# Optimization experiments

Hardware: AMD Instinct MI355X
Metric: run time of the kernel (lower is better)

Reference implementation:

```python
import jax, jax.numpy as jnp
import numpy as np

N_HEAD = 16


def setup_inputs() -> dict:
    key = jax.random.key(0)
    ks = jax.random.split(key, 3)
    B, T, C = 4, 2048, 1024
    x = jax.random.normal(ks[0], (B, T, C), dtype=jnp.float32)
    w_attn = jax.random.normal(ks[1], (3 * C, C), dtype=jnp.float32) * (1.0 / np.sqrt(C))
    b_attn = jnp.zeros((3 * C,), dtype=jnp.float32)
    w_proj = jax.random.normal(ks[2], (C, C), dtype=jnp.float32) * (1.0 / np.sqrt(C))
    b_proj = jnp.zeros((C,), dtype=jnp.float32)
    return {"x": x, "w_attn": w_attn, "b_attn": b_attn, "w_proj": w_proj, "b_proj": b_proj}


def reference(x, w_attn, b_attn, w_proj, b_proj):
    B, T, C = x.shape
    H = N_HEAD
    D = C // H
    qkv = x @ w_attn.T + b_attn                      # [B, T, 3C]
    q, k, v = jnp.split(qkv, 3, axis=-1)
    # [B, T, C] -> [B, H, T, D]
    q = q.reshape(B, T, H, D).transpose(0, 2, 1, 3)
    k = k.reshape(B, T, H, D).transpose(0, 2, 1, 3)
    v = v.reshape(B, T, H, D).transpose(0, 2, 1, 3)
    scale = 1.0 / np.sqrt(D).astype(np.float32)
    att = jnp.einsum('bhqd,bhkd->bhqk', q, k) * scale  # [B, H, T, T]
    causal = jnp.tril(jnp.ones((T, T), dtype=bool))
    att = jnp.where(causal[None, None], att, -jnp.inf)
    att = jax.nn.softmax(att, axis=-1)
    y = jnp.einsum('bhqk,bhkd->bhqd', att, v)          # [B, H, T, D]
    y = y.transpose(0, 2, 1, 3).reshape(B, T, C)
    return y @ w_proj.T + b_proj
```

## Files before the change

kernel.cpp:

```cpp
#include <hip/hip_runtime.h>
#include <hip/hip_bf16.h>
#include <stdint.h>

typedef __attribute__((ext_vector_type(8))) short bf16x8;
typedef __attribute__((ext_vector_type(8))) unsigned short ushort8;
typedef __attribute__((ext_vector_type(4))) float f32x4;

#define MFMA16(a, b, c) __builtin_amdgcn_mfma_f32_16x16x32_bf16((a), (b), (c), 0, 0, 0)

__device__ __forceinline__ unsigned short f2bf(float f) {
  unsigned int u = __builtin_bit_cast(unsigned int, f);
  unsigned int r = (u + 0x7fffu + ((u >> 16) & 1u)) >> 16;
  return (unsigned short)r;
}

__device__ __forceinline__ void gload16(const unsigned short* g, unsigned short* lds_dst) {
  __builtin_amdgcn_global_load_lds(
      (const __attribute__((address_space(1))) unsigned int*)g,
      (__attribute__((address_space(3))) unsigned int*)lds_dst, 16, 0, 0);
}

__global__ void cvt_all(const float* __restrict__ x, const float* __restrict__ wa,
                        const float* __restrict__ wp, unsigned short* __restrict__ xb,
                        unsigned short* __restrict__ wab, unsigned short* __restrict__ wpb) {
  const int C0 = 1048576;
  const int C1 = 1441792;
  const int C2 = 1572864;
  int i = blockIdx.x * blockDim.x + threadIdx.x;
  const int stride = gridDim.x * blockDim.x;
  for (; i < C2; i += stride) {
    const float* src; unsigned short* dst; long e;
    if (i < C0)      { src = x;  dst = xb;  e = (long)i * 8; }
    else if (i < C1) { src = wa; dst = wab; e = (long)(i - C0) * 8; }
    else             { src = wp; dst = wpb; e = (long)(i - C1) * 8; }
    float4 v0 = *(const float4*)(src + e);
    float4 v1 = *(const float4*)(src + e + 4);
    ushort8 o;
    o[0] = f2bf(v0.x); o[1] = f2bf(v0.y); o[2] = f2bf(v0.z); o[3] = f2bf(v0.w);
    o[4] = f2bf(v1.x); o[5] = f2bf(v1.y); o[6] = f2bf(v1.z); o[7] = f2bf(v1.w);
    *(ushort8*)(dst + e) = o;
  }
}

template <int EPI, int NB>
__global__ __launch_bounds__(512, 2)
void gemm_bt(const unsigned short* __restrict__ A,
             const unsigned short* __restrict__ Bt,
             const float* __restrict__ bias,
             int M, int N, int K,
             unsigned short* __restrict__ q_out,
             unsigned short* __restrict__ k_out,
             unsigned short* __restrict__ vt_out,
             float* __restrict__ f_out) {
  constexpr int BNT = NB * 64;
  alignas(16) __shared__ unsigned short Alds[2][2][128 * 64];
  alignas(16) __shared__ unsigned short Blds[2][BNT * 64];
  const int t = threadIdx.x, w = t >> 6, l = t & 63;
  const int bm = blockIdx.x, bn = blockIdx.y;
  const int wm = w >> 2, wn = w & 3;
  const int lo = l & 15, hi = l >> 4, swk = lo & 7;

  f32x4 acc[8][NB];
  const f32x4 zero = {0.f, 0.f, 0.f, 0.f};
#pragma unroll
  for (int i = 0; i < 8; ++i)
#pragma unroll
    for (int j = 0; j < NB; ++j) acc[i][j] = zero;

  const int sr = t >> 3;
  const int gsrcE = ((t & 7) ^ (sr & 7)) * 8;
  const unsigned short* Asrc = A + (long)(bm * 256 + sr) * K + gsrcE;
  const unsigned short* Bsrc = Bt + (long)(bn * BNT + sr) * K + gsrcE;

#define STAGE_AH(sb, qh, koff) do {                                    \
    unsigned short* d_ = &Alds[sb][qh][w * 512];                       \
    const unsigned short* s_ = Asrc + (long)(qh) * 64 * K + (koff);    \
    gload16(s_, d_); gload16(s_ + 128L * K, d_ + 4096); } while (0)
#define STAGE_B(sb, koff) do {                                         \
    _Pragma("unroll")                                                  \
    for (int c_ = 0; c_ < NB; ++c_)                                    \
      gload16(Bsrc + (long)c_ * 64 * K + (koff),                       \
              &Blds[sb][c_ * 4096 + w * 512]); } while (0)

  STAGE_AH(0, 0, 0);
  STAGE_B(0, 0);
  STAGE_AH(0, 1, 0);
  asm volatile("s_waitcnt vmcnt(2)" ::: "memory");
  __builtin_amdgcn_sched_barrier(0);
  __builtin_amdgcn_s_barrier();

  const int lrA = (wm * 64 + lo) * 64;
  const int lrB = (wn * (NB * 16) + lo) * 64;
  const int gk0 = ((hi) ^ swk) * 8;
  const int gk1 = ((4 + hi) ^ swk) * 8;

  bf16x8 af[4][2], blo[2][2], bhi[2];

  for (int kt = 0; kt < 16; ++kt) {
    const int c = kt & 1, nb = c ^ 1;
    const bool st = (kt < 15);
    const int koff = (kt + 1) * 64;
    const unsigned short* A0 = Alds[c][0];
    const unsigned short* A1 = Alds[c][1];
    const unsigned short* Bs = Blds[c];

#pragma unroll
    for (int ii = 0; ii < 4; ++ii) {
      af[ii][0] = *(const bf16x8*)&A0[lrA + ii * 1024 + gk0];
      af[ii][1] = *(const bf16x8*)&A0[lrA + ii * 1024 + gk1];
    }
#pragma unroll
    for (int jj = 0; jj < NB - 1; ++jj) {
      blo[jj][0] = *(const bf16x8*)&Bs[lrB + jj * 1024 + gk0];
      blo[jj][1] = *(const bf16x8*)&Bs[lrB + jj * 1024 + gk1];
    }
    if (st) STAGE_AH(nb, 0, koff);
    __builtin_amdgcn_s_barrier();
    asm volatile("s_waitcnt lgkmcnt(0)" ::: "memory");
    __builtin_amdgcn_sched_barrier(0);
    __builtin_amdgcn_s_setprio(1);
#pragma unroll
    for (int ii = 0; ii < 4; ++ii)
#pragma unroll
      for (int jj = 0; jj < NB - 1; ++jj) {
        acc[ii][jj] = MFMA16(af[ii][0], blo[jj][0], acc[ii][jj]);
        acc[ii][jj] = MFMA16(af[ii][1], blo[jj][1], acc[ii][jj]);
      }
    __builtin_amdgcn_s_setprio(0);
    __builtin_amdgcn_s_barrier();

    bhi[0] = *(const bf16x8*)&Bs[lrB + (NB - 1) * 1024 + gk0];
    bhi[1] = *(const bf16x8*)&Bs[lrB + (NB - 1) * 1024 + gk1];
    if (st) STAGE_B(nb, koff);
    __builtin_amdgcn_s_barrier();
    asm volatile("s_waitcnt lgkmcnt(0)" ::: "memory");
    __builtin_amdgcn_sched_barrier(0);
    __builtin_amdgcn_s_setprio(1);
#pragma unroll
    for (int ii = 0; ii < 4; ++ii) {
      acc[ii][NB - 1] = MFMA16(af[ii][0], bhi[0], acc[ii][NB - 1]);
      acc[ii][NB - 1] = MFMA16(af[ii][1], bhi[1], acc[ii][NB - 1]);
    }
    __builtin_amdgcn_s_setprio(0);
    if (st) {
      if constexpr (NB == 3) { asm volatile("s_waitcnt vmcnt(5)" ::: "memory"); }
      else                   { asm volatile("s_waitcnt vmcnt(4)" ::: "memory"); }
    } else {
      asm volatile("s_waitcnt vmcnt(0)" ::: "memory");
    }
    __builtin_amdgcn_sched_barrier(0);
    __builtin_amdgcn_s_barrier();

#pragma unroll
    for (int ii = 0; ii < 4; ++ii) {
      af[ii][0] = *(const bf16x8*)&A1[lrA + ii * 1024 + gk0];
      af[ii][1] = *(const bf16x8*)&A1[lrA + ii * 1024 + gk1];
    }
    if (st) STAGE_AH(nb, 1, koff);
    __builtin_amdgcn_s_barrier();
    asm volatile("s_waitcnt lgkmcnt(0)" ::: "memory");
    __builtin_amdgcn_sched_barrier(0);
    __builtin_amdgcn_s_setprio(1);
#pragma unroll
    for (int ii = 0; ii < 4; ++ii) {
      acc[4 + ii][NB - 1] = MFMA16(af[ii][0], bhi[0], acc[4 + ii][NB - 1]);
      acc[4 + ii][NB - 1] = MFMA16(af[ii][1], bhi[1], acc[4 + ii][NB - 1]);
    }
    __builtin_amdgcn_s_setprio(0);
    __builtin_amdgcn_s_barrier();

    __builtin_amdgcn_s_setprio(1);
#pragma unroll
    for (int ii = 0; ii < 4; ++ii)
#pragma unroll
      for (int jj = 0; jj < NB - 1; ++jj) {
        acc[4 + ii][jj] = MFMA16(af[ii][0], blo[jj][0], acc[4 + ii][jj]);
        acc[4 + ii][jj] = MFMA16(af[ii][1], blo[jj][1], acc[4 + ii][jj]);
      }
    __builtin_amdgcn_s_setprio(0);
    if (st) {
      asm volatile("s_waitcnt vmcnt(2)" ::: "memory");
      __builtin_amdgcn_sched_barrier(0);
    }
    __builtin_amdgcn_s_barrier();
  }
#undef STAGE_AH
#undef STAGE_B

  if (EPI == 0) {
    constexpr int SCW = 200;
    unsigned short* sc = (unsigned short*)&Alds[0][0][0];
#pragma unroll
    for (int i = 0; i < 8; ++i)
#pragma unroll
      for (int j = 0; j < NB; ++j)
#pragma unroll
        for (int r = 0; r < 4; ++r) {
          int rl = wm * 128 + i * 16 + hi * 4 + r;
          int cl = wn * (NB * 16) + j * 16 + lo;
          int colg = bn * BNT + cl;
          float v = acc[i][j][r] + bias[colg];
          if ((colg >> 10) == 0) v *= 0.1803368801111f;
          sc[rl * SCW + cl] = f2bf(v);
        }
    __syncthreads();
    for (int g = 0; g < NB * 4; ++g) {
      const int cbase = bn * BNT + g * 16;
      const int seg = cbase >> 10;
      const int cc = cbase & 1023;
      const int h = cc >> 6;
      if (seg < 2) {
        const int rl = t >> 1, hf = t & 1;
        bf16x8 vrow = *(const bf16x8*)&sc[rl * SCW + g * 16 + hf * 8];
        int rowg = bm * 256 + rl;
        int b = rowg >> 11, tt = rowg & 2047;
        int d = (cc & 63) + hf * 8;
        long bh = (long)(b * 16 + h);
        unsigned short* outp = (seg == 0 ? q_out : k_out);
        *(bf16x8*)&outp[(bh * 2048 + tt) * 64 + d] = vrow;
      } else {
        const int cl = g * 16 + (t & 15);
        const int r0 = (t >> 4) * 8;
        ushort8 pk;
#pragma unroll
        for (int k2 = 0; k2 < 8; ++k2) pk[k2] = sc[(r0 + k2) * SCW + cl];
        int rowg = bm * 256 + r0;
        int b = rowg >> 11, tt = rowg & 2047;
        int d = (cc & 63) + (t & 15);
        long bh = (long)(b * 16 + h);
        *(ushort8*)&vt_out[(bh * 64 + d) * 2048 + tt] = pk;
      }
    }
  } else {
#pragma unroll
    for (int i = 0; i < 8; ++i) {
#pragma unroll
      for (int j = 0; j < NB; ++j) {
#pragma unroll
        for (int r = 0; r < 4; ++r) {
          int row = bm * 256 + wm * 128 + i * 16 + hi * 4 + r;
          int col = bn * BNT + wn * (NB * 16) + j * 16 + lo;
          float v = acc[i][j][r] + bias[col];
          f_out[(long)row * N + col] = v;
        }
      }
    }
  }
}

__global__ __launch_bounds__(512, 6)
void attn_kernel(const unsigned short* __restrict__ Q,
                 const unsigned short* __restrict__ K,
                 const unsigned short* __restrict__ Vt,
                 unsigned short* __restrict__ Y) {
  alignas(16) __shared__ unsigned short Kbuf[2][64 * 64];
  alignas(16) __shared__ unsigned short Vbuf[2][64 * 64];
  alignas(16) __shared__ unsigned short pbuf[8][16 * 64];
  const int t = threadIdx.x, w = t >> 6, l = t & 63;
  const int lo = l & 15, hi = l >> 4;
  const int bh = blockIdx.x;
  const int s = 15 - blockIdx.y;
  const int b = bh >> 4, h = bh & 15;
  const int nTot = 2 * s + 2;
  const unsigned short* Qp = Q + (long)bh * 2048 * 64;
  const unsigned short* Kp = K + (long)bh * 2048 * 64;
  const unsigned short* Vp = Vt + (long)bh * 64 * 2048;
  unsigned short* pw = pbuf[w];

  const short one_bf = (short)0x3F80;
  const bf16x8 ones = {one_bf, one_bf, one_bf, one_bf, one_bf, one_bf, one_bf, one_bf};
  const f32x4 zero = {0.f, 0.f, 0.f, 0.f};

  const int qb = s * 128 + w * 16;

  bf16x8 qf0, qf1;
  f32x4 lsum;
  f32x4 oacc[4];

  qf0 = *(const bf16x8*)&Qp[(qb + lo) * 64 + hi * 8];
  qf1 = *(const bf16x8*)&Qp[(qb + lo) * 64 + 32 + hi * 8];
  lsum = zero;
#pragma unroll
  for (int dg = 0; dg < 4; ++dg) oacc[dg] = zero;

  const int srow = t >> 3;
  const int scw = ((t & 7) ^ (srow & 7)) * 8;
  const int sw = lo & 7;

#define STAGE(kvoff, bufidx)                                          \
  do {                                                                \
    unsigned short* KB_ = Kbuf[bufidx] + w * 512;                     \
    unsigned short* VB_ = Vbuf[bufidx] + w * 512;                     \
    gload16(Kp + (long)((kvoff) + srow) * 64 + scw, KB_);             \
    gload16(Vp + (long)srow * 2048 + (kvoff) + scw, VB_);             \
  } while (0)

  STAGE(0, 0);
  __syncthreads();

  for (int g = 0; g < nTot; ++g) {
    const int kvb = g * 64;
    const int cur = g & 1;
    if (g + 1 < nTot) {
      STAGE((g + 1) * 64, cur ^ 1);
    }
    if (kvb <= qb + 15) {
      const unsigned short* KB = Kbuf[cur];
      const unsigned short* VB = Vbuf[cur];
      f32x4 sc[4];
#pragma unroll
      for (int cg = 0; cg < 4; ++cg) sc[cg] = zero;
      __builtin_amdgcn_s_setprio(1);
#pragma unroll
      for (int cg = 0; cg < 4; ++cg) {
        bf16x8 k0 = *(const bf16x8*)&KB[(cg * 16 + lo) * 64 + ((hi) ^ sw) * 8];
        bf16x8 k1 = *(const bf16x8*)&KB[(cg * 16 + lo) * 64 + ((4 + hi) ^ sw) * 8];
        sc[cg] = MFMA16(k0, qf0, sc[cg]);
        sc[cg] = MFMA16(k1, qf1, sc[cg]);
      }
      __builtin_amdgcn_s_setprio(0);
      if (kvb + 63 > qb) {
        const int limit = qb + lo - kvb;
#pragma unroll
        for (int cg = 0; cg < 4; ++cg)
#pragma unroll
          for (int r = 0; r < 4; ++r)
            if (cg * 16 + hi * 4 + r > limit) sc[cg][r] = -__builtin_inff();
      }
#pragma unroll
      for (int cg = 0; cg < 4; ++cg) {
        float p0 = exp2f(sc[cg][0]);
        float p1 = exp2f(sc[cg][1]);
        float p2 = exp2f(sc[cg][2]);
        float p3 = exp2f(sc[cg][3]);
        unsigned int u0, u1;
        asm("v_cvt_pk_bf16_f32 %0, %1, %2" : "=v"(u0) : "v"(p0), "v"(p1));
        asm("v_cvt_pk_bf16_f32 %0, %1, %2" : "=v"(u1) : "v"(p2), "v"(p3));
        const int gg = (cg * 2 + (hi >> 1)) ^ sw;
        uint2 val; val.x = u0; val.y = u1;
        *(uint2*)&pw[lo * 64 + gg * 8 + (hi & 1) * 4] = val;
      }
      asm volatile("s_waitcnt lgkmcnt(0)" ::: "memory");
      bf16x8 pa0 = *(const bf16x8*)&pw[lo * 64 + ((hi) ^ sw) * 8];
      bf16x8 pa1 = *(const bf16x8*)&pw[lo * 64 + ((4 + hi) ^ sw) * 8];
      __builtin_amdgcn_s_setprio(1);
      lsum = MFMA16(pa0, ones, lsum);
      lsum = MFMA16(pa1, ones, lsum);
#pragma unroll
      for (int dg = 0; dg < 4; ++dg) {
        bf16x8 vv0 = *(const bf16x8*)&VB[(dg * 16 + lo) * 64 + ((hi) ^ sw) * 8];
        bf16x8 vv1 = *(const bf16x8*)&VB[(dg * 16 + lo) * 64 + ((4 + hi) ^ sw) * 8];
        oacc[dg] = MFMA16(pa0, vv0, oacc[dg]);
        oacc[dg] = MFMA16(pa1, vv1, oacc[dg]);
      }
      __builtin_amdgcn_s_setprio(0);
    }
    __syncthreads();
  }

#pragma unroll
  for (int r = 0; r < 4; ++r) {
    float inv = 1.0f / lsum[r];
    int rowg = qb + hi * 4 + r;
    long base = ((long)b * 2048 + rowg) * 1024 + h * 64;
#pragma unroll
    for (int dg = 0; dg < 4; ++dg)
      Y[base + dg * 16 + lo] = f2bf(oacc[dg][r] * inv);
  }
#undef STAGE
}

extern "C" void kernel_launch(void* const* d_in, const int* in_sizes, int n_in,
                              void* d_out, int out_size, void* d_ws, size_t ws_size,
                              hipStream_t stream) {
  const float* x      = (const float*)d_in[0];
  const float* w_attn = (const float*)d_in[1];
  const float* b_attn = (const float*)d_in[2];
  const float* w_proj = (const float*)d_in[3];
  const float* b_proj = (const float*)d_in[4];
  float* out = (float*)d_out;

  const long NX = 8192L * 1024;
  const long NWA = 3072L * 1024;
  const long NWP = 1024L * 1024;
  const long NQ = 64L * 2048 * 64;

  char* ws = (char*)d_ws;
  unsigned short* xb  = (unsigned short*)ws; ws += NX * 2;
  unsigned short* wab = (unsigned short*)ws; ws += NWA * 2;
  unsigned short* wpb = (unsigned short*)ws; ws += NWP * 2;
  unsigned short* qb  = (unsigned short*)ws; ws += NQ * 2;
  unsigned short* kb  = (unsigned short*)ws; ws += NQ * 2;
  unsigned short* vtb = (unsigned short*)ws; ws += NQ * 2;
  unsigned short* yb  = (unsigned short*)ws; ws += NX * 2;

  cvt_all<<<2048, 256, 0, stream>>>(x, w_attn, w_proj, xb, wab, wpb);

  dim3 g1(32, 16);
  gemm_bt<0, 3><<<g1, 512, 0, stream>>>(xb, wab, b_attn, 8192, 3072, 1024,
                                        qb, kb, vtb, nullptr);
  dim3 ga(64, 16);
  attn_kernel<<<ga, 512, 0, stream>>>(qb, kb, vtb, yb);
  dim3 g2(32, 8);
  gemm_bt<1, 2><<<g2, 512, 0, stream>>>(yb, wpb, b_proj, 8192, 1024, 1024,
                                        nullptr, nullptr, nullptr, out);
}
```

Measured before the change: 159.9 us.

## Rewrite attention with 32x32 MFMA, register-resident P via permlane swap

The attention kernel moves from 16x16x32 MFMA tiles with 8 waves of 16 query rows to 32x32x16 MFMA tiles with 4 waves of 32 query rows each. The softmax probabilities stay in registers and are reshuffled with v_permlane32_swap instead of round-tripping through an LDS buffer. The row sum is computed with VALU adds rather than an extra MFMA against a ones vector. The output goes through an LDS staging buffer so Y is written with 16-byte vector stores. In exchange, per-thread register pressure rises, blocks are half the size, and causal masking now skips work at a coarser 32-key granularity.

```diff
diff --git a/kernel.cpp b/kernel.cpp
--- a/kernel.cpp
+++ b/kernel.cpp
@@ -5,8 +5,11 @@
 typedef __attribute__((ext_vector_type(8))) short bf16x8;
 typedef __attribute__((ext_vector_type(8))) unsigned short ushort8;
 typedef __attribute__((ext_vector_type(4))) float f32x4;
+typedef __attribute__((ext_vector_type(16))) float f32x16;
+typedef __attribute__((ext_vector_type(4))) unsigned int u32x4;
 
 #define MFMA16(a, b, c) __builtin_amdgcn_mfma_f32_16x16x32_bf16((a), (b), (c), 0, 0, 0)
+#define MFMA32(a, b, c) __builtin_amdgcn_mfma_f32_32x32x16_bf16((a), (b), (c), 0, 0, 0)
 
 __device__ __forceinline__ unsigned short f2bf(float f) {
   unsigned int u = __builtin_bit_cast(unsigned int, f);
@@ -248,16 +251,16 @@
   }
 }
 
-__global__ __launch_bounds__(512, 6)
+__global__ __launch_bounds__(256, 4)
 void attn_kernel(const unsigned short* __restrict__ Q,
                  const unsigned short* __restrict__ K,
                  const unsigned short* __restrict__ Vt,
                  unsigned short* __restrict__ Y) {
   alignas(16) __shared__ unsigned short Kbuf[2][64 * 64];
   alignas(16) __shared__ unsigned short Vbuf[2][64 * 64];
-  alignas(16) __shared__ unsigned short pbuf[8][16 * 64];
+  alignas(16) __shared__ unsigned short obuf[4][32 * 72];
   const int t = threadIdx.x, w = t >> 6, l = t & 63;
-  const int lo = l & 15, hi = l >> 4;
+  const int q5 = l & 31, hi5 = l >> 5, sw = l & 7;
   const int bh = blockIdx.x;
   const int s = 15 - blockIdx.y;
   const int b = bh >> 4, h = bh & 15;
@@ -265,34 +268,32 @@
   const unsigned short* Qp = Q + (long)bh * 2048 * 64;
   const unsigned short* Kp = K + (long)bh * 2048 * 64;
   const unsigned short* Vp = Vt + (long)bh * 64 * 2048;
-  unsigned short* pw = pbuf[w];
-
-  const short one_bf = (short)0x3F80;
-  const bf16x8 ones = {one_bf, one_bf, one_bf, one_bf, one_bf, one_bf, one_bf, one_bf};
-  const f32x4 zero = {0.f, 0.f, 0.f, 0.f};
-
-  const int qb = s * 128 + w * 16;
-
-  bf16x8 qf0, qf1;
-  f32x4 lsum;
-  f32x4 oacc[4];
-
-  qf0 = *(const bf16x8*)&Qp[(qb + lo) * 64 + hi * 8];
-  qf1 = *(const bf16x8*)&Qp[(qb + lo) * 64 + 32 + hi * 8];
-  lsum = zero;
-#pragma unroll
-  for (int dg = 0; dg < 4; ++dg) oacc[dg] = zero;
-
-  const int srow = t >> 3;
-  const int scw = ((t & 7) ^ (srow & 7)) * 8;
-  const int sw = lo & 7;
-
-#define STAGE(kvoff, bufidx)                                          \
-  do {                                                                \
-    unsigned short* KB_ = Kbuf[bufidx] + w * 512;                     \
-    unsigned short* VB_ = Vbuf[bufidx] + w * 512;                     \
-    gload16(Kp + (long)((kvoff) + srow) * 64 + scw, KB_);             \
-    gload16(Vp + (long)srow * 2048 + (kvoff) + scw, VB_);             \
+
+  const int qbw = s * 128 + w * 32;
+
+  bf16x8 qf[4];
+#pragma unroll
+  for (int m = 0; m < 4; ++m)
+    qf[m] = *(const bf16x8*)&Qp[(qbw + q5) * 64 + m * 16 + hi5 * 8];
+
+  f32x16 oacc[2];
+#pragma unroll
+  for (int dh = 0; dh < 2; ++dh)
+#pragma unroll
+    for (int r = 0; r < 16; ++r) oacc[dh][r] = 0.f;
+  float lsum = 0.f;
+
+  const int rowk = w * 8 + (l >> 3);
+  const int scw = ((l & 7) ^ (l >> 3)) * 8;
+
+#define STAGE(kvoff, bufidx)                                              \
+  do {                                                                    \
+    unsigned short* KB_ = Kbuf[bufidx] + w * 512;                         \
+    unsigned short* VB_ = Vbuf[bufidx] + w * 512;                         \
+    gload16(Kp + (long)((kvoff) + rowk) * 64 + scw, KB_);                 \
+    gload16(Kp + (long)((kvoff) + 32 + rowk) * 64 + scw, KB_ + 2048);     \
+    gload16(Vp + (long)rowk * 2048 + (kvoff) + scw, VB_);                 \
+    gload16(Vp + (long)(32 + rowk) * 2048 + (kvoff) + scw, VB_ + 2048);   \
   } while (0)
 
   STAGE(0, 0);
@@ -301,71 +302,87 @@
   for (int g = 0; g < nTot; ++g) {
     const int kvb = g * 64;
     const int cur = g & 1;
-    if (g + 1 < nTot) {
-      STAGE((g + 1) * 64, cur ^ 1);
-    }
-    if (kvb <= qb + 15) {
+    if (g + 1 < nTot) STAGE((g + 1) * 64, cur ^ 1);
+    if (kvb <= qbw + 31) {
       const unsigned short* KB = Kbuf[cur];
       const unsigned short* VB = Vbuf[cur];
-      f32x4 sc[4];
-#pragma unroll
-      for (int cg = 0; cg < 4; ++cg) sc[cg] = zero;
-      __builtin_amdgcn_s_setprio(1);
-#pragma unroll
-      for (int cg = 0; cg < 4; ++cg) {
-        bf16x8 k0 = *(const bf16x8*)&KB[(cg * 16 + lo) * 64 + ((hi) ^ sw) * 8];
-        bf16x8 k1 = *(const bf16x8*)&KB[(cg * 16 + lo) * 64 + ((4 + hi) ^ sw) * 8];
-        sc[cg] = MFMA16(k0, qf0, sc[cg]);
-        sc[cg] = MFMA16(k1, qf1, sc[cg]);
+#pragma unroll
+      for (int kt = 0; kt < 2; ++kt) {
+        if (kvb + kt * 32 <= qbw + 31) {
+          f32x16 sacc;
+#pragma unroll
+          for (int r = 0; r < 16; ++r) sacc[r] = 0.f;
+          __builtin_amdgcn_s_setprio(1);
+#pragma unroll
+          for (int m = 0; m < 4; ++m) {
+            bf16x8 kf = *(const bf16x8*)&KB[(kt * 32 + q5) * 64 + ((2 * m + hi5) ^ sw) * 8];
+            sacc = MFMA32(kf, qf[m], sacc);
+          }
+          __builtin_amdgcn_s_setprio(0);
+          if (kvb + kt * 32 + 31 > qbw) {
+            const int lim = qbw + q5 - kvb - kt * 32 - 4 * hi5;
+#pragma unroll
+            for (int r = 0; r < 16; ++r)
+              if (((r & 3) + 8 * (r >> 2)) > lim) sacc[r] = -__builtin_inff();
+          }
+          float p[16];
+#pragma unroll
+          for (int r = 0; r < 16; ++r) p[r] = exp2f(sacc[r]);
+          {
+            float t0 = (p[0] + p[1]) + (p[2] + p[3]);
+            float t1 = (p[4] + p[5]) + (p[6] + p[7]);
+            float t2 = (p[8] + p[9]) + (p[10] + p[11]);
+            float t3 = (p[12] + p[13]) + (p[14] + p[15]);
+            lsum += (t0 + t1) + (t2 + t3);
+          }
+          unsigned int u0, u1, u2, u3, u4, u5, u6, u7;
+          asm("v_cvt_pk_bf16_f32 %0, %1, %2" : "=v"(u0) : "v"(p[0]), "v"(p[1]));
+          asm("v_cvt_pk_bf16_f32 %0, %1, %2" : "=v"(u1) : "v"(p[2]), "v"(p[3]));
+          asm("v_cvt_pk_bf16_f32 %0, %1, %2" : "=v"(u2) : "v"(p[4]), "v"(p[5]));
+          asm("v_cvt_pk_bf16_f32 %0, %1, %2" : "=v"(u3) : "v"(p[6]), "v"(p[7]));
+          asm("v_cvt_pk_bf16_f32 %0, %1, %2" : "=v"(u4) : "v"(p[8]), "v"(p[9]));
+          asm("v_cvt_pk_bf16_f32 %0, %1, %2" : "=v"(u5) : "v"(p[10]), "v"(p[11]));
+          asm("v_cvt_pk_bf16_f32 %0, %1, %2" : "=v"(u6) : "v"(p[12]), "v"(p[13]));
+          asm("v_cvt_pk_bf16_f32 %0, %1, %2" : "=v"(u7) : "v"(p[14]), "v"(p[15]));
+          asm volatile("v_permlane32_swap_b32 %0, %1" : "+v"(u0), "+v"(u2));
+          asm volatile("v_permlane32_swap_b32 %0, %1" : "+v"(u1), "+v"(u3));
+          asm volatile("v_permlane32_swap_b32 %0, %1" : "+v"(u4), "+v"(u6));
+          asm volatile("v_permlane32_swap_b32 %0, %1" : "+v"(u5), "+v"(u7));
+          u32x4 w0 = {u0, u1, u2, u3};
+          u32x4 w1 = {u4, u5, u6, u7};
+          bf16x8 pf0 = __builtin_bit_cast(bf16x8, w0);
+          bf16x8 pf1 = __builtin_bit_cast(bf16x8, w1);
+          __builtin_amdgcn_s_setprio(1);
+#pragma unroll
+          for (int dh = 0; dh < 2; ++dh) {
+            bf16x8 v0 = *(const bf16x8*)&VB[(dh * 32 + q5) * 64 + ((kt * 4 + 0 + hi5) ^ sw) * 8];
+            bf16x8 v1 = *(const bf16x8*)&VB[(dh * 32 + q5) * 64 + ((kt * 4 + 2 + hi5) ^ sw) * 8];
+            oacc[dh] = MFMA32(v0, pf0, oacc[dh]);
+            oacc[dh] = MFMA32(v1, pf1, oacc[dh]);
+          }
+          __builtin_amdgcn_s_setprio(0);
+        }
       }
-      __builtin_amdgcn_s_setprio(0);
-      if (kvb + 63 > qb) {
-        const int limit = qb + lo - kvb;
-#pragma unroll
-        for (int cg = 0; cg < 4; ++cg)
-#pragma unroll
-          for (int r = 0; r < 4; ++r)
-            if (cg * 16 + hi * 4 + r > limit) sc[cg][r] = -__builtin_inff();
-      }
-#pragma unroll
-      for (int cg = 0; cg < 4; ++cg) {
-        float p0 = exp2f(sc[cg][0]);
-        float p1 = exp2f(sc[cg][1]);
-        float p2 = exp2f(sc[cg][2]);
-        float p3 = exp2f(sc[cg][3]);
-        unsigned int u0, u1;
-        asm("v_cvt_pk_bf16_f32 %0, %1, %2" : "=v"(u0) : "v"(p0), "v"(p1));
-        asm("v_cvt_pk_bf16_f32 %0, %1, %2" : "=v"(u1) : "v"(p2), "v"(p3));
-        const int gg = (cg * 2 + (hi >> 1)) ^ sw;
-        uint2 val; val.x = u0; val.y = u1;
-        *(uint2*)&pw[lo * 64 + gg * 8 + (hi & 1) * 4] = val;
-      }
-      asm volatile("s_waitcnt lgkmcnt(0)" ::: "memory");
-      bf16x8 pa0 = *(const bf16x8*)&pw[lo * 64 + ((hi) ^ sw) * 8];
-      bf16x8 pa1 = *(const bf16x8*)&pw[lo * 64 + ((4 + hi) ^ sw) * 8];
-      __builtin_amdgcn_s_setprio(1);
-      lsum = MFMA16(pa0, ones, lsum);
-      lsum = MFMA16(pa1, ones, lsum);
-#pragma unroll
-      for (int dg = 0; dg < 4; ++dg) {
-        bf16x8 vv0 = *(const bf16x8*)&VB[(dg * 16 + lo) * 64 + ((hi) ^ sw) * 8];
-        bf16x8 vv1 = *(const bf16x8*)&VB[(dg * 16 + lo) * 64 + ((4 + hi) ^ sw) * 8];
-        oacc[dg] = MFMA16(pa0, vv0, oacc[dg]);
-        oacc[dg] = MFMA16(pa1, vv1, oacc[dg]);
-      }
-      __builtin_amdgcn_s_setprio(0);
     }
     __syncthreads();
   }
 
-#pragma unroll
-  for (int r = 0; r < 4; ++r) {
-    float inv = 1.0f / lsum[r];
-    int rowg = qb + hi * 4 + r;
-    long base = ((long)b * 2048 + rowg) * 1024 + h * 64;
-#pragma unroll
-    for (int dg = 0; dg < 4; ++dg)
-      Y[base + dg * 16 + lo] = f2bf(oacc[dg][r] * inv);
+  lsum += __shfl_xor(lsum, 32);
+  float inv = 1.0f / lsum;
+  unsigned short* ow = obuf[w];
+#pragma unroll
+  for (int dh = 0; dh < 2; ++dh)
+#pragma unroll
+    for (int r = 0; r < 16; ++r) {
+      int d = dh * 32 + (r & 3) + 8 * (r >> 2) + 4 * hi5;
+      ow[q5 * 72 + d] = f2bf(oacc[dh][r] * inv);
+    }
+  const int orow = l >> 1, och = l & 1;
+  long ybase = ((long)b * 2048 + qbw + orow) * 1024 + h * 64 + och * 32;
+#pragma unroll
+  for (int c = 0; c < 4; ++c) {
+    bf16x8 v = *(const bf16x8*)&ow[orow * 72 + och * 32 + c * 8];
+    *(bf16x8*)&Y[ybase + c * 8] = v;
   }
 #undef STAGE
 }
@@ -400,7 +417,7 @@
   gemm_bt<0, 3><<<g1, 512, 0, stream>>>(xb, wab, b_attn, 8192, 3072, 1024,
                                         qb, kb, vtb, nullptr);
   dim3 ga(64, 16);
-  attn_kernel<<<ga, 512, 0, stream>>>(qb, kb, vtb, yb);
+  attn_kernel<<<ga, 256, 0, stream>>>(qb, kb, vtb, yb);
   dim3 g2(32, 8);
   gemm_bt<1, 2><<<g2, 512, 0, stream>>>(yb, wpb, b_proj, 8192, 1024, 1024,
                                         nullptr, nullptr, nullptr, out);
```

Measured after the change: 169.9 us. 1.06x slower.
